# Performance work log

Hardware: AMD Instinct MI355X
Metric: run time of the kernel (lower is better)

Reference implementation:

```python
import jax, jax.numpy as jnp
import numpy as np

B = 65536
G = 9          # grid_size
C = 10         # num_classes
BS = 3         # block_size = sqrt(grid_size)
CONSTRAINT_WEIGHT = 0.1


def setup_inputs() -> dict:
    key = jax.random.key(0)
    k1, k2, k3 = jax.random.split(key, 3)
    logits = jax.random.normal(k1, (B, G, G, C), dtype=jnp.float32)
    targets = jax.random.randint(k2, (B, G, G), 0, C)
    puzzles = jax.random.randint(k3, (B, G, G), 0, C)
    return {"logits": logits, "targets": targets, "puzzles": puzzles}


def _sudoku_loss(logits, targets, puzzles):
    mask = (puzzles == 0).astype(logits.dtype)               # [B, G, G]

    # --- masked cross-entropy over empty cells ---
    logp = jax.nn.log_softmax(logits, axis=-1)               # [B, G, G, C]
    ce = -jnp.take_along_axis(logp, targets[..., None], axis=-1)[..., 0]
    ce_loss = (ce * mask).sum() / (mask.sum() + 1e-8)

    # --- constraint loss (rows, cols, 3x3 boxes), fully vectorized ---
    probs = jnp.exp(logp)                                    # softmax probs
    wp = probs * mask[..., None]                             # [B, G, G, C]

    def group_mse(digit_sums, msum):
        # digit_sums: [B, G_groups, C]; msum: [B, G_groups]
        # torch: per-group F.mse_loss over [B, C-1], summed over groups
        target = msum[..., None] / G                         # [B, Gg, 1]
        diff = digit_sums[..., 1:] - target                  # [B, Gg, C-1]
        return (diff * diff).mean(axis=(0, 2)).sum()

    # rows: sum over columns (axis 2)
    row_loss = group_mse(wp.sum(axis=2), mask.sum(axis=2))
    # cols: sum over rows (axis 1)
    col_loss = group_mse(wp.sum(axis=1), mask.sum(axis=1))
    # boxes: reshape to [B, bi, ri, bj, cj, C], sum within-box dims
    box_ds = wp.reshape(B, BS, BS, BS, BS, C).sum(axis=(2, 4)).reshape(B, G, C)
    box_ms = mask.reshape(B, BS, BS, BS, BS).sum(axis=(2, 4)).reshape(B, G)
    box_loss = group_mse(box_ds, box_ms)

    num_constraints = G * 2 + BS * BS                        # 27
    constraint_loss = (row_loss + col_loss + box_loss) / num_constraints

    # torch wraps the constraint loss in torch.tensor(...), detaching it
    total = ce_loss + CONSTRAINT_WEIGHT * jax.lax.stop_gradient(constraint_loss)
    return total, ce_loss, constraint_loss


def reference(logits, targets, puzzles):
    total, ce_loss, constraint_loss = _sudoku_loss(logits, targets, puzzles)
    return total, ce_loss, constraint_loss
```

## Files before the change

### kernel.cpp

```cpp
#include <hip/hip_runtime.h>


constexpr int kB = 65536;
constexpr int kPuzzPerWave  = 7;
constexpr int kWavesPerBlk  = 4;
constexpr int kPuzzPerBlk   = kPuzzPerWave * kWavesPerBlk;
constexpr int kBlocks       = (kB + kPuzzPerBlk - 1) / kPuzzPerBlk;

__global__ __launch_bounds__(256) void sudoku_main(
    const float* __restrict__ logits,
    const int*   __restrict__ targets,
    const int*   __restrict__ puzzles,
    float*       __restrict__ ws)
{
    __shared__ float colacc[kPuzzPerBlk * 90];
    __shared__ float red[kWavesPerBlk][3];

    const int tid = threadIdx.x;
    #pragma unroll
    for (int i = tid; i < kPuzzPerBlk * 90; i += 256) colacc[i] = 0.f;
    __syncthreads();

    const int wave = tid >> 6;
    const int lane = tid & 63;
    const int plw  = lane / 9;
    const int r    = lane - plw * 9;
    const int pLoc = wave * kPuzzPerWave + plw;
    const int p    = blockIdx.x * kPuzzPerBlk + pLoc;

    const bool active = (plw < kPuzzPerWave) && (p < kB);

    float ce = 0.f, rowm = 0.f, diff2 = 0.f;
    float rowsum[9];
    float boxp[3][9];
    float bm[3] = {0.f, 0.f, 0.f};
    #pragma unroll
    for (int c = 0; c < 9; ++c) rowsum[c] = 0.f;
    #pragma unroll
    for (int b = 0; b < 3; ++b)
        #pragma unroll
        for (int c = 0; c < 9; ++c) boxp[b][c] = 0.f;

    if (active) {
        const float* lg = logits  + (size_t)p * 810 + r * 90;
        const int*   tg = targets + (size_t)p * 81  + r * 9;
        const int*   pz = puzzles + (size_t)p * 81  + r * 9;

        int pzv[9], tgv[9];
        #pragma unroll
        for (int j = 0; j < 9; ++j) pzv[j] = pz[j];
        #pragma unroll
        for (int j = 0; j < 9; ++j) tgv[j] = tg[j];

        float* colrow = &colacc[pLoc * 90];

        #pragma unroll
        for (int j = 0; j < 9; ++j) {
            const float* xp = lg + j * 10;
            float x[10];
            #pragma unroll
            for (int h = 0; h < 5; ++h) {
                const float2 v = *(const float2*)(xp + 2 * h);
                x[2 * h] = v.x; x[2 * h + 1] = v.y;
            }
            float mx = x[0];
            #pragma unroll
            for (int c = 1; c < 10; ++c) mx = fmaxf(mx, x[c]);
            float e[10], S = 0.f;
            #pragma unroll
            for (int c = 0; c < 10; ++c) { e[c] = __expf(x[c] - mx); S += e[c]; }
            const float inv = 1.f / S;
            const float lse = __logf(S);

            const int t = tgv[j];
            float xt = x[0];
            #pragma unroll
            for (int c = 1; c < 10; ++c) xt = (t == c) ? x[c] : xt;

            const float maskf = (pzv[j] == 0) ? 1.f : 0.f;
            ce   += maskf * (mx + lse - xt);
            rowm += maskf;
            const int jb = j / 3;
            bm[jb] += maskf;

            const float winv = inv * maskf;
            float w[9];
            #pragma unroll
            for (int c = 1; c < 10; ++c) {
                w[c - 1] = e[c] * winv;
                rowsum[c - 1]   += w[c - 1];
                boxp[jb][c - 1] += w[c - 1];
            }
            if (pzv[j] == 0) {
                float* cb = colrow + j * 10;
                atomicAdd(&cb[0], 1.f);
                #pragma unroll
                for (int c = 1; c < 10; ++c) atomicAdd(&cb[c], w[c - 1]);
            }
        }

        const float tr = rowm * (1.f / 9.f);
        #pragma unroll
        for (int c = 0; c < 9; ++c) { const float d = rowsum[c] - tr; diff2 += d * d; }

        const bool boxLead = (r == 0) || (r == 3) || (r == 6);
        #pragma unroll
        for (int bj = 0; bj < 3; ++bj) {
            float bmm = bm[bj];
            bmm += __shfl_down(bm[bj], 1);
            bmm += __shfl_down(bm[bj], 2);
            const float tb = bmm * (1.f / 9.f);
            #pragma unroll
            for (int c = 0; c < 9; ++c) {
                float bs = boxp[bj][c];
                bs += __shfl_down(boxp[bj][c], 1);
                bs += __shfl_down(boxp[bj][c], 2);
                const float d = bs - tb;
                diff2 += boxLead ? d * d : 0.f;
            }
        }
    }

    __syncthreads();

    if (active) {
        const float* cb = &colacc[pLoc * 90 + r * 10];
        const float tc = cb[0] * (1.f / 9.f);
        #pragma unroll
        for (int c = 1; c < 10; ++c) { const float d = cb[c] - tc; diff2 += d * d; }
    }

    #pragma unroll
    for (int off = 32; off > 0; off >>= 1) {
        diff2 += __shfl_down(diff2, off);
        ce    += __shfl_down(ce, off);
        rowm  += __shfl_down(rowm, off);
    }
    if (lane == 0) { red[wave][0] = diff2; red[wave][1] = ce; red[wave][2] = rowm; }
    __syncthreads();
    if (tid == 0) {
        float d = 0.f, c2 = 0.f, m = 0.f;
        #pragma unroll
        for (int wv = 0; wv < kWavesPerBlk; ++wv) {
            d += red[wv][0]; c2 += red[wv][1]; m += red[wv][2];
        }
        const int b = blockIdx.x;
        ws[b]               = d;
        ws[kBlocks + b]     = c2;
        ws[2 * kBlocks + b] = m;
    }
}

__global__ __launch_bounds__(256) void sudoku_final(
    const float* __restrict__ ws, float* __restrict__ out)
{
    __shared__ float red[4][3];
    float s0 = 0.f, s1 = 0.f, s2 = 0.f;
    for (int i = threadIdx.x; i < kBlocks; i += 256) {
        s0 += ws[i];
        s1 += ws[kBlocks + i];
        s2 += ws[2 * kBlocks + i];
    }
    #pragma unroll
    for (int off = 32; off > 0; off >>= 1) {
        s0 += __shfl_down(s0, off);
        s1 += __shfl_down(s1, off);
        s2 += __shfl_down(s2, off);
    }
    const int wave = threadIdx.x >> 6;
    if ((threadIdx.x & 63) == 0) { red[wave][0] = s0; red[wave][1] = s1; red[wave][2] = s2; }
    __syncthreads();
    if (threadIdx.x == 0) {
        float d = 0.f, c2 = 0.f, m = 0.f;
        #pragma unroll
        for (int wv = 0; wv < 4; ++wv) { d += red[wv][0]; c2 += red[wv][1]; m += red[wv][2]; }
        const float ce_loss    = c2 / (m + 1e-8f);
        const float constraint = d / ((float)kB * 9.f * 27.f);
        out[0] = ce_loss + 0.1f * constraint;
        out[1] = ce_loss;
        out[2] = constraint;
    }
}

extern "C" void kernel_launch(void* const* d_in, const int* in_sizes, int n_in,
                              void* d_out, int out_size, void* d_ws, size_t ws_size,
                              hipStream_t stream)
{
    const float* logits  = (const float*)d_in[0];
    const int*   targets = (const int*)d_in[1];
    const int*   puzzles = (const int*)d_in[2];
    float* ws  = (float*)d_ws;
    float* out = (float*)d_out;

    sudoku_main<<<kBlocks, 256, 0, stream>>>(logits, targets, puzzles, ws);
    sudoku_final<<<1, 256, 0, stream>>>(ws, out);
}
```

Baseline: 361.9 us.

## Map one thread per cell and accumulate row/col/box sums via LDS atomics

Replaces the one-thread-per-row mapping, which kept row and box sums in registers and combined boxes with shuffles, with one thread per cell. Each block now handles 3 puzzles (243 of 256 threads active), and each cell adds its probabilities into row, column and box accumulators in shared memory with atomics. Loads become fully coalesced per cell, and only masked cells read targets and logits. The cost is about 30 LDS atomics per masked cell, heavy contention on those atomics, and about 21.8k small blocks. The final reduction is also widened to 1024 threads.

```diff
diff --git a/kernel.cpp b/kernel.cpp
--- a/kernel.cpp
+++ b/kernel.cpp
@@ -2,10 +2,8 @@
 
 
 constexpr int kB = 65536;
-constexpr int kPuzzPerWave  = 7;
-constexpr int kWavesPerBlk  = 4;
-constexpr int kPuzzPerBlk   = kPuzzPerWave * kWavesPerBlk;
-constexpr int kBlocks       = (kB + kPuzzPerBlk - 1) / kPuzzPerBlk;
+constexpr int kPuzzPerBlk = 3;
+constexpr int kBlocks = (kB + kPuzzPerBlk - 1) / kPuzzPerBlk;
 
 __global__ __launch_bounds__(256) void sudoku_main(
     const float* __restrict__ logits,
@@ -13,50 +11,26 @@
     const int*   __restrict__ puzzles,
     float*       __restrict__ ws)
 {
-    __shared__ float colacc[kPuzzPerBlk * 90];
-    __shared__ float red[kWavesPerBlk][3];
+    __shared__ float acc[kPuzzPerBlk][27][10];
+    __shared__ float red[4][3];
 
     const int tid = threadIdx.x;
-    #pragma unroll
-    for (int i = tid; i < kPuzzPerBlk * 90; i += 256) colacc[i] = 0.f;
+    for (int i = tid; i < kPuzzPerBlk * 270; i += 256) ((float*)acc)[i] = 0.f;
     __syncthreads();
 
-    const int wave = tid >> 6;
-    const int lane = tid & 63;
-    const int plw  = lane / 9;
-    const int r    = lane - plw * 9;
-    const int pLoc = wave * kPuzzPerWave + plw;
-    const int p    = blockIdx.x * kPuzzPerBlk + pLoc;
+    float ce = 0.f, mcnt = 0.f, diff2 = 0.f;
 
-    const bool active = (plw < kPuzzPerWave) && (p < kB);
+    const int q    = tid / 81;
+    const int cell = tid - q * 81;
+    const int p    = blockIdx.x * kPuzzPerBlk + q;
+    const bool valid = (tid < 243) && (p < kB);
 
-    float ce = 0.f, rowm = 0.f, diff2 = 0.f;
-    float rowsum[9];
-    float boxp[3][9];
-    float bm[3] = {0.f, 0.f, 0.f};
-    #pragma unroll
-    for (int c = 0; c < 9; ++c) rowsum[c] = 0.f;
-    #pragma unroll
-    for (int b = 0; b < 3; ++b)
-        #pragma unroll
-        for (int c = 0; c < 9; ++c) boxp[b][c] = 0.f;
-
-    if (active) {
-        const float* lg = logits  + (size_t)p * 810 + r * 90;
-        const int*   tg = targets + (size_t)p * 81  + r * 9;
-        const int*   pz = puzzles + (size_t)p * 81  + r * 9;
-
-        int pzv[9], tgv[9];
-        #pragma unroll
-        for (int j = 0; j < 9; ++j) pzv[j] = pz[j];
-        #pragma unroll
-        for (int j = 0; j < 9; ++j) tgv[j] = tg[j];
-
-        float* colrow = &colacc[pLoc * 90];
-
-        #pragma unroll
-        for (int j = 0; j < 9; ++j) {
-            const float* xp = lg + j * 10;
+    if (valid) {
+        const size_t base = (size_t)p * 81 + cell;
+        const int pz = puzzles[base];
+        if (pz == 0) {
+            const int t = targets[base];
+            const float* xp = logits + base * 10;
             float x[10];
             #pragma unroll
             for (int h = 0; h < 5; ++h) {
@@ -72,78 +46,57 @@
             const float inv = 1.f / S;
             const float lse = __logf(S);
 
-            const int t = tgv[j];
             float xt = x[0];
             #pragma unroll
             for (int c = 1; c < 10; ++c) xt = (t == c) ? x[c] : xt;
+            ce   += mx + lse - xt;
+            mcnt += 1.f;
 
-            const float maskf = (pzv[j] == 0) ? 1.f : 0.f;
-            ce   += maskf * (mx + lse - xt);
-            rowm += maskf;
-            const int jb = j / 3;
-            bm[jb] += maskf;
-
-            const float winv = inv * maskf;
-            float w[9];
+            const int r  = cell / 9;
+            const int cj = cell - r * 9;
+            const int bx = (r / 3) * 3 + (cj / 3);
+            float* rowa = acc[q][r];
+            float* cola = acc[q][9 + cj];
+            float* boxa = acc[q][18 + bx];
+            atomicAdd(&rowa[0], 1.f);
+            atomicAdd(&cola[0], 1.f);
+            atomicAdd(&boxa[0], 1.f);
             #pragma unroll
             for (int c = 1; c < 10; ++c) {
-                w[c - 1] = e[c] * winv;
-                rowsum[c - 1]   += w[c - 1];
-                boxp[jb][c - 1] += w[c - 1];
-            }
-            if (pzv[j] == 0) {
-                float* cb = colrow + j * 10;
-                atomicAdd(&cb[0], 1.f);
-                #pragma unroll
-                for (int c = 1; c < 10; ++c) atomicAdd(&cb[c], w[c - 1]);
-            }
-        }
-
-        const float tr = rowm * (1.f / 9.f);
-        #pragma unroll
-        for (int c = 0; c < 9; ++c) { const float d = rowsum[c] - tr; diff2 += d * d; }
-
-        const bool boxLead = (r == 0) || (r == 3) || (r == 6);
-        #pragma unroll
-        for (int bj = 0; bj < 3; ++bj) {
-            float bmm = bm[bj];
-            bmm += __shfl_down(bm[bj], 1);
-            bmm += __shfl_down(bm[bj], 2);
-            const float tb = bmm * (1.f / 9.f);
-            #pragma unroll
-            for (int c = 0; c < 9; ++c) {
-                float bs = boxp[bj][c];
-                bs += __shfl_down(boxp[bj][c], 1);
-                bs += __shfl_down(boxp[bj][c], 2);
-                const float d = bs - tb;
-                diff2 += boxLead ? d * d : 0.f;
+                const float w = e[c] * inv;
+                atomicAdd(&rowa[c], w);
+                atomicAdd(&cola[c], w);
+                atomicAdd(&boxa[c], w);
             }
         }
     }
-
     __syncthreads();
 
-    if (active) {
-        const float* cb = &colacc[pLoc * 90 + r * 10];
-        const float tc = cb[0] * (1.f / 9.f);
-        #pragma unroll
-        for (int c = 1; c < 10; ++c) { const float d = cb[c] - tc; diff2 += d * d; }
+    if (tid < kPuzzPerBlk * 27) {
+        const int q2 = tid / 27;
+        const int g  = tid - q2 * 27;
+        if (blockIdx.x * kPuzzPerBlk + q2 < kB) {
+            const float* a = acc[q2][g];
+            const float tg = a[0] * (1.f / 9.f);
+            #pragma unroll
+            for (int c = 1; c < 10; ++c) { const float d = a[c] - tg; diff2 += d * d; }
+        }
     }
 
     #pragma unroll
     for (int off = 32; off > 0; off >>= 1) {
         diff2 += __shfl_down(diff2, off);
         ce    += __shfl_down(ce, off);
-        rowm  += __shfl_down(rowm, off);
+        mcnt  += __shfl_down(mcnt, off);
     }
-    if (lane == 0) { red[wave][0] = diff2; red[wave][1] = ce; red[wave][2] = rowm; }
+    const int wave = tid >> 6;
+    const int lane = tid & 63;
+    if (lane == 0) { red[wave][0] = diff2; red[wave][1] = ce; red[wave][2] = mcnt; }
     __syncthreads();
     if (tid == 0) {
         float d = 0.f, c2 = 0.f, m = 0.f;
         #pragma unroll
-        for (int wv = 0; wv < kWavesPerBlk; ++wv) {
-            d += red[wv][0]; c2 += red[wv][1]; m += red[wv][2];
-        }
+        for (int wv = 0; wv < 4; ++wv) { d += red[wv][0]; c2 += red[wv][1]; m += red[wv][2]; }
         const int b = blockIdx.x;
         ws[b]               = d;
         ws[kBlocks + b]     = c2;
@@ -151,12 +104,12 @@
     }
 }
 
-__global__ __launch_bounds__(256) void sudoku_final(
+__global__ __launch_bounds__(1024) void sudoku_final(
     const float* __restrict__ ws, float* __restrict__ out)
 {
-    __shared__ float red[4][3];
+    __shared__ float red[16][3];
     float s0 = 0.f, s1 = 0.f, s2 = 0.f;
-    for (int i = threadIdx.x; i < kBlocks; i += 256) {
+    for (int i = threadIdx.x; i < kBlocks; i += 1024) {
         s0 += ws[i];
         s1 += ws[kBlocks + i];
         s2 += ws[2 * kBlocks + i];
@@ -173,7 +126,7 @@
     if (threadIdx.x == 0) {
         float d = 0.f, c2 = 0.f, m = 0.f;
         #pragma unroll
-        for (int wv = 0; wv < 4; ++wv) { d += red[wv][0]; c2 += red[wv][1]; m += red[wv][2]; }
+        for (int wv = 0; wv < 16; ++wv) { d += red[wv][0]; c2 += red[wv][1]; m += red[wv][2]; }
         const float ce_loss    = c2 / (m + 1e-8f);
         const float constraint = d / ((float)kB * 9.f * 27.f);
         out[0] = ce_loss + 0.1f * constraint;
@@ -193,5 +146,5 @@
     float* out = (float*)d_out;
 
     sudoku_main<<<kBlocks, 256, 0, stream>>>(logits, targets, puzzles, ws);
-    sudoku_final<<<1, 256, 0, stream>>>(ws, out);
+    sudoku_final<<<1, 1024, 0, stream>>>(ws, out);
 }
```

Result: slower. 369.1 us (+2.0%).
